# Kernel optimization log

Measured on AMD Instinct MI355X. Metric: run time of the kernel, lower is better.

## Reference

```python
import jax, jax.numpy as jnp
import numpy as np

B, C_IN, N, F_OUT = 16, 128, 2048, 64
NEG_SLOPE = 0.33
MASK_VAL = -9e15


def setup_inputs() -> dict:
    key = jax.random.key(0)
    k1, k2, k3, k4 = jax.random.split(key, 4)
    h = jax.random.normal(k1, (B, C_IN, N, 1), dtype=jnp.float32)
    g = jax.random.normal(k2, (B, 1, N, N), dtype=jnp.float32)
    # xavier_uniform with gain=1.414
    gain = 1.414
    lim_W = gain * np.sqrt(6.0 / (C_IN + F_OUT))
    W = jax.random.uniform(k3, (C_IN, F_OUT), minval=-lim_W, maxval=lim_W, dtype=jnp.float32)
    lim_a = gain * np.sqrt(6.0 / (2 * F_OUT + 1))
    a = jax.random.uniform(k4, (2 * F_OUT, 1), minval=-lim_a, maxval=lim_a, dtype=jnp.float32)
    return {"h": h, "g": g, "W": W, "a": a}


def reference(h, g, W, a):
    # h: [B, C, N, 1] -> node features [B, N, C]
    hn = jnp.transpose(h[..., 0], (0, 2, 1))
    Wh = jnp.einsum('bnc,cf->bnf', hn, W)  # [B, N, F]
    F = W.shape[1]
    a1, a2 = a[:F, 0], a[F:, 0]
    # additive attention: e[i,j] = leakyrelu(Wh[i]@a1 + Wh[j]@a2)
    e = jax.nn.leaky_relu((Wh @ a1)[:, :, None] + (Wh @ a2)[:, None, :], NEG_SLOPE)  # [B,N,N]
    mask = g[:, 0] > 0  # [B, N, N]
    attn = jax.nn.softmax(jnp.where(mask, e, MASK_VAL), axis=-1)
    h_prime = jnp.einsum('bij,bjf->bif', attn, Wh)  # [B, N, F]
    return jnp.transpose(h_prime, (0, 2, 1))[..., None]  # [B, F, N, 1]
```

## Files before the change

kernel.cpp:

```cpp
#include <hip/hip_runtime.h>
#include <hip/hip_bf16.h>

#define NB 16
#define NC 128
#define NN 2048
#define NF 64
#define NEG_SLOPE 0.33f

typedef float    f32x4 __attribute__((ext_vector_type(4)));
typedef _Float16 f16x4 __attribute__((ext_vector_type(4)));
typedef _Float16 f16x8 __attribute__((ext_vector_type(8)));

__device__ __forceinline__ float lrelu(float x) {
    return fmaxf(x, x * NEG_SLOPE);
}

__global__ __launch_bounds__(256) void k_precompute(
    const float* __restrict__ h, const float* __restrict__ W,
    const float* __restrict__ a, _Float16* __restrict__ wht,
    float* __restrict__ s1g, float* __restrict__ s2g)
{
    __shared__ float Wl[64 * 64];
    __shared__ float ht[64 * 129];

    const int t = threadIdx.x;
    const int b = blockIdx.x >> 5;
    const int n0 = (blockIdx.x & 31) << 6;
    const int lane = t & 63, cg = t >> 6;

    #pragma unroll 8
    for (int k = 0; k < 32; ++k) {
        const int c = cg * 32 + k;
        ht[lane * 129 + c] = h[(size_t)(b * NC + c) * NN + n0 + lane];
    }

    const int fg = t & 15, ns = t >> 4;
    f32x4 acc[4] = {};
    for (int half = 0; half < 2; ++half) {
        if (half) __syncthreads();
        #pragma unroll
        for (int k = 0; k < 4; ++k) {
            const int idx = k * 1024 + t * 4;
            *(f32x4*)&Wl[idx] = *(const f32x4*)&W[half * 4096 + idx];
        }
        __syncthreads();
        #pragma unroll 4
        for (int c2 = 0; c2 < 64; ++c2) {
            const f32x4 wv = *(const f32x4*)&Wl[c2 * 64 + fg * 4];
            #pragma unroll
            for (int m = 0; m < 4; ++m) {
                const float hv = ht[(ns * 4 + m) * 129 + half * 64 + c2];
                acc[m] += wv * hv;
            }
        }
    }

    const f32x4 a1v = *(const f32x4*)&a[fg * 4];
    const f32x4 a2v = *(const f32x4*)&a[NF + fg * 4];
    #pragma unroll
    for (int m = 0; m < 4; ++m) {
        float p1 = acc[m].x * a1v.x + acc[m].y * a1v.y + acc[m].z * a1v.z + acc[m].w * a1v.w;
        float p2 = acc[m].x * a2v.x + acc[m].y * a2v.y + acc[m].z * a2v.z + acc[m].w * a2v.w;
        #pragma unroll
        for (int d = 1; d < 16; d <<= 1) {
            p1 += __shfl_xor(p1, d, 64);
            p2 += __shfl_xor(p2, d, 64);
        }
        if (fg == 0) {
            const int n = n0 + ns * 4 + m;
            s1g[(size_t)b * NN + n] = p1;
            s2g[(size_t)b * NN + n] = p2;
        }
    }
    #pragma unroll
    for (int q = 0; q < 4; ++q) {
        f16x4 v;
        v[0] = (_Float16)acc[0][q]; v[1] = (_Float16)acc[1][q];
        v[2] = (_Float16)acc[2][q]; v[3] = (_Float16)acc[3][q];
        const int f = fg * 4 + q;
        *(f16x4*)&wht[((size_t)b * NF + f) * NN + n0 + ns * 4] = v;
    }
}

__global__ __launch_bounds__(512, 4) void k_attn(
    const float* __restrict__ g, const _Float16* __restrict__ wht,
    const float* __restrict__ s1g, const float* __restrict__ s2g,
    float* __restrict__ out)
{
    __shared__ float s2b[NN];
    __shared__ float s1b[64];
    __shared__ float wred[8];
    __shared__ float SrowP[2][4][16];
    __shared__ f32x4 accS[4][4][64];

    const int t = threadIdx.x;
    const int lane = t & 63;
    const int w = t >> 6;
    const int rg = w & 3, jq = w >> 2;
    const int b = blockIdx.x >> 5;
    const int i0 = (blockIdx.x & 31) << 6;

    const f32x4 s2v = *(const f32x4*)&s2g[(size_t)b * NN + t * 4];
    *(f32x4*)&s2b[t * 4] = s2v;
    if (t < 64) s1b[t] = s1g[(size_t)b * NN + i0 + t];
    float lm = fmaxf(fmaxf(s2v.x, s2v.y), fmaxf(s2v.z, s2v.w));
    #pragma unroll
    for (int d = 1; d < 64; d <<= 1) lm = fmaxf(lm, __shfl_xor(lm, d, 64));
    if (lane == 0) wred[w] = lm;
    __syncthreads();
    float S2MAX = wred[0];
    #pragma unroll
    for (int q = 1; q < 8; ++q) S2MAX = fmaxf(S2MAX, wred[q]);

    const int row = lane & 15;
    const int kg = lane >> 4;
    const float s1r = s1b[rg * 16 + row];
    const float M = lrelu(s1r + S2MAX);

    const float* gp = g + (size_t)b * NN * NN
                      + (size_t)(i0 + rg * 16 + row) * NN + jq * 1024 + kg * 8;
    const _Float16* wp0 = wht + ((size_t)b * NF + row) * NN + jq * 1024 + kg * 8;
    const _Float16* wp1 = wp0 + (size_t)16 * NN;
    const _Float16* wp2 = wp0 + (size_t)32 * NN;
    const _Float16* wp3 = wp0 + (size_t)48 * NN;
    const float* s2p = &s2b[jq * 1024 + kg * 8];

    f32x4 acc0 = {0,0,0,0}, acc1 = {0,0,0,0}, acc2 = {0,0,0,0}, acc3 = {0,0,0,0};
    float su = 0.0f;

    f32x4 ga = *(const f32x4*)(gp);
    f32x4 gb = *(const f32x4*)(gp + 4);
    f16x8 w0 = *(const f16x8*)(wp0);
    f16x8 w1 = *(const f16x8*)(wp1);
    f16x8 w2 = *(const f16x8*)(wp2);
    f16x8 w3 = *(const f16x8*)(wp3);

    #pragma unroll 1
    for (int ch = 0; ch < 32; ++ch) {
        f32x4 nga = ga, ngb = gb;
        f16x8 nw0 = w0, nw1 = w1, nw2 = w2, nw3 = w3;
        if (ch < 31) {
            const int o = (ch + 1) * 32;
            nga = *(const f32x4*)(gp + o);
            ngb = *(const f32x4*)(gp + o + 4);
            nw0 = *(const f16x8*)(wp0 + o);
            nw1 = *(const f16x8*)(wp1 + o);
            nw2 = *(const f16x8*)(wp2 + o);
            nw3 = *(const f16x8*)(wp3 + o);
        }
        const f32x4 sv0 = *(const f32x4*)(s2p + ch * 32);
        const f32x4 sv1 = *(const f32x4*)(s2p + ch * 32 + 4);

        f16x8 af;
        #pragma unroll
        for (int u = 0; u < 4; ++u) {
            const float q0 = (ga[u] > 0.0f) ? __expf(lrelu(s1r + sv0[u]) - M) : 0.0f;
            su += q0;
            af[u] = (_Float16)q0;
            const float q1 = (gb[u] > 0.0f) ? __expf(lrelu(s1r + sv1[u]) - M) : 0.0f;
            su += q1;
            af[u + 4] = (_Float16)q1;
        }
        acc0 = __builtin_amdgcn_mfma_f32_16x16x32_f16(af, w0, acc0, 0, 0, 0);
        acc1 = __builtin_amdgcn_mfma_f32_16x16x32_f16(af, w1, acc1, 0, 0, 0);
        acc2 = __builtin_amdgcn_mfma_f32_16x16x32_f16(af, w2, acc2, 0, 0, 0);
        acc3 = __builtin_amdgcn_mfma_f32_16x16x32_f16(af, w3, acc3, 0, 0, 0);
        ga = nga; gb = ngb; w0 = nw0; w1 = nw1; w2 = nw2; w3 = nw3;
    }

    su += __shfl_xor(su, 16, 64);
    su += __shfl_xor(su, 32, 64);
    if (lane < 16) SrowP[jq][rg][lane] = su;
    if (jq == 1) {
        accS[rg][0][lane] = acc0;
        accS[rg][1][lane] = acc1;
        accS[rg][2][lane] = acc2;
        accS[rg][3][lane] = acc3;
    }
    __syncthreads();
    if (jq == 0) {
        acc0 += accS[rg][0][lane];
        acc1 += accS[rg][1][lane];
        acc2 += accS[rg][2][lane];
        acc3 += accS[rg][3][lane];
        float rinv[4];
        #pragma unroll
        for (int r = 0; r < 4; ++r) {
            const int ri = kg * 4 + r;
            rinv[r] = 1.0f / (SrowP[0][rg][ri] + SrowP[1][rg][ri]);
        }
        const int ibase = i0 + rg * 16 + kg * 4;
        f32x4 o0, o1, o2, o3;
        #pragma unroll
        for (int r = 0; r < 4; ++r) {
            o0[r] = acc0[r] * rinv[r];
            o1[r] = acc1[r] * rinv[r];
            o2[r] = acc2[r] * rinv[r];
            o3[r] = acc3[r] * rinv[r];
        }
        *(f32x4*)&out[((size_t)b * NF + row) * NN + ibase] = o0;
        *(f32x4*)&out[((size_t)b * NF + 16 + row) * NN + ibase] = o1;
        *(f32x4*)&out[((size_t)b * NF + 32 + row) * NN + ibase] = o2;
        *(f32x4*)&out[((size_t)b * NF + 48 + row) * NN + ibase] = o3;
    }
}

extern "C" void kernel_launch(void* const* d_in, const int* in_sizes, int n_in,
                              void* d_out, int out_size, void* d_ws, size_t ws_size,
                              hipStream_t stream)
{
    (void)in_sizes; (void)n_in; (void)out_size; (void)ws_size;
    const float* h = (const float*)d_in[0];
    const float* g = (const float*)d_in[1];
    const float* W = (const float*)d_in[2];
    const float* a = (const float*)d_in[3];
    float* out = (float*)d_out;

    char* ws = (char*)d_ws;
    _Float16* wht = (_Float16*)ws;
    float* s1 = (float*)(ws + (size_t)NB * NF * NN * sizeof(_Float16));
    float* s2 = s1 + (size_t)NB * NN;

    k_precompute<<<NB * (NN / 64), 256, 0, stream>>>(h, W, a, wht, s1, s2);
    k_attn<<<NB * (NN / 64), 512, 0, stream>>>(g, wht, s1, s2, out);
}
```

Before: 112.7 us.

## Restructure attention kernel: per-wave full-row sweep, LDS-staged probabilities, MFMA row sums

```diff
diff --git a/kernel.cpp b/kernel.cpp
--- a/kernel.cpp
+++ b/kernel.cpp
@@ -6,13 +6,18 @@
 #define NN 2048
 #define NF 64
 #define NEG_SLOPE 0.33f
-
+#define EXP_K 1.4426950408889634f
+
+typedef float    f32x2 __attribute__((ext_vector_type(2)));
 typedef float    f32x4 __attribute__((ext_vector_type(4)));
 typedef _Float16 f16x4 __attribute__((ext_vector_type(4)));
 typedef _Float16 f16x8 __attribute__((ext_vector_type(8)));
 
 __device__ __forceinline__ float lrelu(float x) {
     return fmaxf(x, x * NEG_SLOPE);
+}
+__device__ __forceinline__ float rdfl(float v) {
+    return __int_as_float(__builtin_amdgcn_readfirstlane(__float_as_int(v)));
 }
 
 __global__ __launch_bounds__(256) void k_precompute(
@@ -82,127 +87,126 @@
     }
 }
 
-__global__ __launch_bounds__(512, 4) void k_attn(
+__global__ __launch_bounds__(256, 4) void k_attn(
     const float* __restrict__ g, const _Float16* __restrict__ wht,
     const float* __restrict__ s1g, const float* __restrict__ s2g,
     float* __restrict__ out)
 {
     __shared__ float s2b[NN];
     __shared__ float s1b[64];
-    __shared__ float wred[8];
-    __shared__ float SrowP[2][4][16];
-    __shared__ f32x4 accS[4][4][64];
+    __shared__ float wred[4];
+    __shared__ __align__(16) _Float16 Pc[4][1024];
 
     const int t = threadIdx.x;
     const int lane = t & 63;
     const int w = t >> 6;
-    const int rg = w & 3, jq = w >> 2;
-    const int b = blockIdx.x >> 5;
-    const int i0 = (blockIdx.x & 31) << 6;
-
-    const f32x4 s2v = *(const f32x4*)&s2g[(size_t)b * NN + t * 4];
-    *(f32x4*)&s2b[t * 4] = s2v;
-    if (t < 64) s1b[t] = s1g[(size_t)b * NN + i0 + t];
-    float lm = fmaxf(fmaxf(s2v.x, s2v.y), fmaxf(s2v.z, s2v.w));
+
+    const int p = blockIdx.x;
+    const int b = (p & 7) + ((p >> 8) << 3);
+    const int strip = (p >> 3) & 31;
+    const int i0 = strip * 64 + w * 16;
+
+    f32x4 sA = *(const f32x4*)&s2g[(size_t)b * NN + t * 8];
+    f32x4 sB = *(const f32x4*)&s2g[(size_t)b * NN + t * 8 + 4];
+    sA *= EXP_K; sB *= EXP_K;
+    *(f32x4*)&s2b[t * 8] = sA;
+    *(f32x4*)&s2b[t * 8 + 4] = sB;
+    if (t < 64) s1b[t] = s1g[(size_t)b * NN + strip * 64 + t] * EXP_K;
+    float lm = fmaxf(fmaxf(fmaxf(sA.x, sA.y), fmaxf(sA.z, sA.w)),
+                     fmaxf(fmaxf(sB.x, sB.y), fmaxf(sB.z, sB.w)));
     #pragma unroll
     for (int d = 1; d < 64; d <<= 1) lm = fmaxf(lm, __shfl_xor(lm, d, 64));
     if (lane == 0) wred[w] = lm;
     __syncthreads();
-    float S2MAX = wred[0];
-    #pragma unroll
-    for (int q = 1; q < 8; ++q) S2MAX = fmaxf(S2MAX, wred[q]);
-
-    const int row = lane & 15;
-    const int kg = lane >> 4;
-    const float s1r = s1b[rg * 16 + row];
-    const float M = lrelu(s1r + S2MAX);
-
-    const float* gp = g + (size_t)b * NN * NN
-                      + (size_t)(i0 + rg * 16 + row) * NN + jq * 1024 + kg * 8;
-    const _Float16* wp0 = wht + ((size_t)b * NF + row) * NN + jq * 1024 + kg * 8;
-    const _Float16* wp1 = wp0 + (size_t)16 * NN;
-    const _Float16* wp2 = wp0 + (size_t)32 * NN;
-    const _Float16* wp3 = wp0 + (size_t)48 * NN;
-    const float* s2p = &s2b[jq * 1024 + kg * 8];
+    const float S2MAX = fmaxf(fmaxf(wred[0], wred[1]), fmaxf(wred[2], wred[3]));
+
+    float s1r[16], M[16];
+    #pragma unroll
+    for (int r = 0; r < 16; ++r) {
+        const float v = s1b[w * 16 + r];
+        s1r[r] = rdfl(v);
+        M[r]   = rdfl(lrelu(v + S2MAX));
+    }
+
+    const float* gp = g + (size_t)b * NN * NN + (size_t)i0 * NN + lane;
+    const int fc = lane & 15, kg = lane >> 4;
+    const _Float16* wb = wht + ((size_t)b * NF + fc) * NN + kg * 8;
+    char* pcb = (char*)&Pc[w][0];
 
     f32x4 acc0 = {0,0,0,0}, acc1 = {0,0,0,0}, acc2 = {0,0,0,0}, acc3 = {0,0,0,0};
-    float su = 0.0f;
-
-    f32x4 ga = *(const f32x4*)(gp);
-    f32x4 gb = *(const f32x4*)(gp + 4);
-    f16x8 w0 = *(const f16x8*)(wp0);
-    f16x8 w1 = *(const f16x8*)(wp1);
-    f16x8 w2 = *(const f16x8*)(wp2);
-    f16x8 w3 = *(const f16x8*)(wp3);
+    f32x4 acc_s = {0,0,0,0};
+    f16x8 ones;
+    #pragma unroll
+    for (int u = 0; u < 8; ++u) ones[u] = (_Float16)1.0f;
+
+    float ga[16], gb[16];
+    #pragma unroll
+    for (int r = 0; r < 16; ++r) ga[r] = gp[(size_t)r * NN];
+
+#define CHUNK_BODY(CH, CUR, NXT)                                               \
+    {                                                                          \
+                                           \
+        f16x8 bfv[2][4];                                                       \
+        _Pragma("unroll")                                                      \
+        for (int ks = 0; ks < 2; ++ks) {                                       \
+            _Pragma("unroll")                                                  \
+            for (int ft = 0; ft < 4; ++ft)                                     \
+                bfv[ks][ft] = *(const f16x8*)(wb + (size_t)ft * 16 * NN        \
+                                              + (CH) * 64 + ks * 32);          \
+        }                                                                      \
+        __builtin_amdgcn_sched_barrier(0);                                     \
+                                            \
+        if ((CH) < 31) {                                                       \
+            _Pragma("unroll")                                                  \
+            for (int r = 0; r < 16; ++r)                                       \
+                NXT[r] = gp[(size_t)r * NN + ((CH) + 1) * 64];                 \
+        }                                                                      \
+        __builtin_amdgcn_sched_barrier(0);                                     \
+               \
+        const float sv = s2b[(CH) * 64 + lane];                                \
+        _Pragma("unroll")                                                      \
+        for (int r = 0; r < 16; ++r) {                                         \
+            const float arg = lrelu(s1r[r] + sv) - M[r];                       \
+            const float pe  = (CUR[r] > 0.0f) ? __builtin_amdgcn_exp2f(arg) : 0.0f; \
+            *(_Float16*)(pcb + ((r * 128 + lane * 2) ^ ((r & 7) << 4))) = (_Float16)pe; \
+        }                                                                      \
+                            \
+        _Pragma("unroll")                                                      \
+        for (int ks = 0; ks < 2; ++ks) {                                       \
+            const f16x8 af = *(const f16x8*)(pcb +                             \
+                ((fc * 128 + ks * 64 + kg * 16) ^ ((fc & 7) << 4)));           \
+            acc0  = __builtin_amdgcn_mfma_f32_16x16x32_f16(af, bfv[ks][0], acc0, 0, 0, 0); \
+            acc1  = __builtin_amdgcn_mfma_f32_16x16x32_f16(af, bfv[ks][1], acc1, 0, 0, 0); \
+            acc2  = __builtin_amdgcn_mfma_f32_16x16x32_f16(af, bfv[ks][2], acc2, 0, 0, 0); \
+            acc3  = __builtin_amdgcn_mfma_f32_16x16x32_f16(af, bfv[ks][3], acc3, 0, 0, 0); \
+            acc_s = __builtin_amdgcn_mfma_f32_16x16x32_f16(af, ones,       acc_s, 0, 0, 0); \
+        }                                                                      \
+    }
 
     #pragma unroll 1
-    for (int ch = 0; ch < 32; ++ch) {
-        f32x4 nga = ga, ngb = gb;
-        f16x8 nw0 = w0, nw1 = w1, nw2 = w2, nw3 = w3;
-        if (ch < 31) {
-            const int o = (ch + 1) * 32;
-            nga = *(const f32x4*)(gp + o);
-            ngb = *(const f32x4*)(gp + o + 4);
-            nw0 = *(const f16x8*)(wp0 + o);
-            nw1 = *(const f16x8*)(wp1 + o);
-            nw2 = *(const f16x8*)(wp2 + o);
-            nw3 = *(const f16x8*)(wp3 + o);
-        }
-        const f32x4 sv0 = *(const f32x4*)(s2p + ch * 32);
-        const f32x4 sv1 = *(const f32x4*)(s2p + ch * 32 + 4);
-
-        f16x8 af;
-        #pragma unroll
-        for (int u = 0; u < 4; ++u) {
-            const float q0 = (ga[u] > 0.0f) ? __expf(lrelu(s1r + sv0[u]) - M) : 0.0f;
-            su += q0;
-            af[u] = (_Float16)q0;
-            const float q1 = (gb[u] > 0.0f) ? __expf(lrelu(s1r + sv1[u]) - M) : 0.0f;
-            su += q1;
-            af[u + 4] = (_Float16)q1;
-        }
-        acc0 = __builtin_amdgcn_mfma_f32_16x16x32_f16(af, w0, acc0, 0, 0, 0);
-        acc1 = __builtin_amdgcn_mfma_f32_16x16x32_f16(af, w1, acc1, 0, 0, 0);
-        acc2 = __builtin_amdgcn_mfma_f32_16x16x32_f16(af, w2, acc2, 0, 0, 0);
-        acc3 = __builtin_amdgcn_mfma_f32_16x16x32_f16(af, w3, acc3, 0, 0, 0);
-        ga = nga; gb = ngb; w0 = nw0; w1 = nw1; w2 = nw2; w3 = nw3;
-    }
-
-    su += __shfl_xor(su, 16, 64);
-    su += __shfl_xor(su, 32, 64);
-    if (lane < 16) SrowP[jq][rg][lane] = su;
-    if (jq == 1) {
-        accS[rg][0][lane] = acc0;
-        accS[rg][1][lane] = acc1;
-        accS[rg][2][lane] = acc2;
-        accS[rg][3][lane] = acc3;
-    }
-    __syncthreads();
-    if (jq == 0) {
-        acc0 += accS[rg][0][lane];
-        acc1 += accS[rg][1][lane];
-        acc2 += accS[rg][2][lane];
-        acc3 += accS[rg][3][lane];
-        float rinv[4];
-        #pragma unroll
-        for (int r = 0; r < 4; ++r) {
-            const int ri = kg * 4 + r;
-            rinv[r] = 1.0f / (SrowP[0][rg][ri] + SrowP[1][rg][ri]);
-        }
-        const int ibase = i0 + rg * 16 + kg * 4;
-        f32x4 o0, o1, o2, o3;
-        #pragma unroll
-        for (int r = 0; r < 4; ++r) {
-            o0[r] = acc0[r] * rinv[r];
-            o1[r] = acc1[r] * rinv[r];
-            o2[r] = acc2[r] * rinv[r];
-            o3[r] = acc3[r] * rinv[r];
-        }
-        *(f32x4*)&out[((size_t)b * NF + row) * NN + ibase] = o0;
-        *(f32x4*)&out[((size_t)b * NF + 16 + row) * NN + ibase] = o1;
-        *(f32x4*)&out[((size_t)b * NF + 32 + row) * NN + ibase] = o2;
-        *(f32x4*)&out[((size_t)b * NF + 48 + row) * NN + ibase] = o3;
-    }
+    for (int it = 0; it < 16; ++it) {
+        CHUNK_BODY(it * 2,     ga, gb);
+        CHUNK_BODY(it * 2 + 1, gb, ga);
+    }
+#undef CHUNK_BODY
+
+    f32x4 rinv;
+    #pragma unroll
+    for (int q = 0; q < 4; ++q) rinv[q] = 1.0f / acc_s[q];
+
+    const size_t ob = ((size_t)b * NF + fc) * NN + (size_t)i0 + kg * 4;
+    f32x4 o0, o1, o2, o3;
+    #pragma unroll
+    for (int q = 0; q < 4; ++q) {
+        o0[q] = acc0[q] * rinv[q];
+        o1[q] = acc1[q] * rinv[q];
+        o2[q] = acc2[q] * rinv[q];
+        o3[q] = acc3[q] * rinv[q];
+    }
+    *(f32x4*)&out[ob]                   = o0;
+    *(f32x4*)&out[ob + (size_t)16 * NN] = o1;
+    *(f32x4*)&out[ob + (size_t)32 * NN] = o2;
+    *(f32x4*)&out[ob + (size_t)48 * NN] = o3;
 }
 
 extern "C" void kernel_launch(void* const* d_in, const int* in_sizes, int n_in,
@@ -222,5 +226,5 @@
     float* s2 = s1 + (size_t)NB * NN;
 
     k_precompute<<<NB * (NN / 64), 256, 0, stream>>>(h, W, a, wht, s1, s2);
-    k_attn<<<NB * (NN / 64), 512, 0, stream>>>(g, wht, s1, s2, out);
-}
+    k_attn<<<NB * (NN / 64), 256, 0, stream>>>(g, wht, s1, s2, out);
+}
```

Result: faster. 94.02 us (-16.5%).
